# Optimization experiments

Hardware: AMD Instinct MI355X
Metric: run time of the kernel (lower is better)

Reference implementation:

```python
import jax, jax.numpy as jnp
import numpy as np
from jax import lax

DN = ('NCHW', 'OIHW', 'NCHW')

def conv(x, k):
    return lax.conv_general_dilated(x, k, (1, 1), 'SAME', dimension_numbers=DN)

def conv_adj(y, k):
    # adjoint of SAME stride-1 conv: correlate with spatially-flipped, channel-transposed kernel
    return conv(y, jnp.flip(k, (2, 3)).transpose(1, 0, 2, 3))

def setup_inputs() -> dict:
    key = jax.random.key(0)
    ks = jax.random.split(key, 8)
    B, H, W = 8, 512, 512
    Cw, Ch = 4, 32
    return {
        'sino': jax.random.normal(ks[0], (B, 1, H, W), jnp.float32),
        'x': jax.random.normal(ks[1], (B, 1, H, W), jnp.float32),
        'laam': jnp.asarray([0.05], jnp.float32),
        'miu': jnp.asarray([0.01], jnp.float32),
        'Kw': jax.random.normal(ks[2], (Cw, 1, 3, 3), jnp.float32) * 0.1,
        'Ka': jax.random.normal(ks[3], (1, 1, 5, 5), jnp.float32) * 0.1,
        'W1': jax.random.normal(ks[4], (Ch, 1, 3, 3), jnp.float32) * 0.05,
        'b1': jnp.zeros((Ch,), jnp.float32),
        'W2': jax.random.normal(ks[5], (Ch, Ch, 3, 3), jnp.float32) * 0.05,
        'b2': jnp.zeros((Ch,), jnp.float32),
        'W3': jax.random.normal(ks[6], (1, Ch, 3, 3), jnp.float32) * 0.05,
        'b3': jnp.zeros((1,), jnp.float32),
    }

def reference(sino, x, laam, miu, Kw, Ka, W1, b1, W2, b2, W3, b3):
    mu = miu  # shape (1,), broadcasts as scalar

    def Wop(u):  return conv(u, Kw)          # analysis transform, [B,Cw,H,W]
    def WTop(v): return conv_adj(v, Kw)      # synthesis (adjoint)
    def Aop(u):  return conv(u, Ka)          # system operator surrogate
    def ATop(s): return conv_adj(s, Ka)

    def cnn(u):
        h = jax.nn.relu(conv(u, W1) + b1[None, :, None, None])
        h = jax.nn.relu(conv(h, W2) + b2[None, :, None, None])
        return u + conv(h, W3) + b3[None, :, None, None]

    def AWx(p):  # (A^T A + mu W^T W) p
        return ATop(Aop(p)) + mu * WTop(Wop(p))

    # --- MetaInvH forward ---
    Wu = Wop(x)
    dnz = jax.nn.relu(Wu - laam) - jax.nn.relu(-Wu - laam)  # soft threshold
    rhs = ATop(sino) + WTop(dnz) * miu
    uk0 = cnn(x)
    res = AWx(uk0) - rhs

    # --- CG_alg, 5 iterations + final half step ---
    xk, r, p = uk0, res, -res
    for _ in range(5):
        Ap = Aop(p)                                   # [B,1,H,W]
        Wp = Wop(p)                                   # [B,Cw,H,W]
        pATAp = jnp.sum(Ap * Ap, axis=(1, 2, 3))      # [B]
        pWTWp = mu * jnp.sum(Wp * Wp, axis=(1, 2, 3)) # [B]
        rTr = jnp.sum(r * r, axis=(1, 2, 3))
        al = (rTr / (pWTWp + pATAp))[:, None, None, None]
        xk = xk + al * p
        r = r + al * (ATop(Ap) + mu * WTop(Wp))
        be = (jnp.sum(r * r, axis=(1, 2, 3)) / rTr)[:, None, None, None]
        p = -r + be * p
    Ap = Aop(p)
    Wp = Wop(p)
    pATAp = jnp.sum(Ap * Ap, axis=(1, 2, 3))
    pWTWp = mu * jnp.sum(Wp * Wp, axis=(1, 2, 3))
    rTr = jnp.sum(r * r, axis=(1, 2, 3))
    al = (rTr / (pWTWp + pATAp))[:, None, None, None]
    return xk + al * p
```

## Files before the change

### kernel.cpp

```cpp
#include <hip/hip_runtime.h>

#define HH 512
#define WW 512
#define BB 8
#define IMG (HH*WW)
#define NTOT (BB*IMG)

typedef float f32x4 __attribute__((ext_vector_type(4)));
typedef _Float16 half8 __attribute__((ext_vector_type(8)));

__device__ inline uint f2h2(float a, float b) {
  uint d; asm("v_cvt_pkrtz_f16_f32 %0, %1, %2" : "=v"(d) : "v"(a), "v"(b)); return d;
}
__device__ inline uint pkfma(uint a, uint b, uint c) {
  uint d; asm("v_pk_fma_f16 %0, %1, %2, %3" : "=v"(d) : "v"(a), "v"(b), "v"(c)); return d;
}
__device__ inline uint pkmax0(uint a) {
  uint d, z = 0u; asm("v_pk_max_f16 %0, %1, %2" : "=v"(d) : "v"(a), "v"(z)); return d;
}

__device__ inline void atomic_block_sum(float part, float* red, float* dst) {
  for (int off = 32; off > 0; off >>= 1) part += __shfl_down(part, off, 64);
  int lane = threadIdx.x & 63, w = threadIdx.x >> 6;
  if (lane == 0) red[w] = part;
  __syncthreads();
  if (threadIdx.x == 0) atomicAdd(dst, red[0] + red[1] + red[2] + red[3]);
}

__device__ inline bool mA5(int t, int e) {
  return (t==0) ? (e<=2) : (t==1) ? (e<=3) : (t==3) ? (e>=1) : (t==4) ? (e>=2) : true;
}
__device__ inline bool mW3(int t, int e) {
  return (t==0) ? (e<=1) : (t==4) ? (e>=1) : true;
}

__global__ void k_prep(const float* __restrict__ Ka, const float* __restrict__ Kw,
                       const float* __restrict__ miu,
                       const float* __restrict__ W1, const float* __restrict__ b1,
                       const float* __restrict__ W2, const float* __restrict__ W3,
                       float* __restrict__ tab, ushort* __restrict__ w2pk,
                       uint* __restrict__ w1pk, uint* __restrict__ b1pk,
                       ushort* __restrict__ w3fr, float* __restrict__ scal) {
  __shared__ float lka[25], lkw[36], lw1[288], lw3[288];
  int tid = threadIdx.x;
  if (tid < 192) scal[tid] = 0.f;
  if (tid < 25) lka[tid] = Ka[tid];
  if (tid < 36) lkw[tid] = Kw[tid];
  if (tid < 288) { lw1[tid] = W1[tid]; lw3[tid] = W3[tid]; }
  __syncthreads();
  const float mu = miu[0];
  #pragma unroll
  for (int k = 0; k < 2; k++) {
    int idx = tid + k*1024;
    if (idx < 2025) {
      int c = idx / 81, o = idx - c*81;
      int ty = c / 5, tx = c - 5*ty;
      int uy = o / 9 - 4, ux = o % 9 - 4;
      float s = 0.f;
      for (int ey = 0; ey < 5; ey++)
        for (int ex = 0; ex < 5; ex++) {
          int dy = ey + uy, dx = ex + ux;
          if (dy >= 0 && dy < 5 && dx >= 0 && dx < 5 && mA5(ty,ey) && mA5(tx,ex))
            s += lka[ey*5+ex] * lka[dy*5+dx];
        }
      float sw = 0.f;
      for (int ch = 0; ch < 4; ch++)
        for (int ey = 0; ey < 3; ey++)
          for (int ex = 0; ex < 3; ex++) {
            int dy = ey + uy, dx = ex + ux;
            if (dy >= 0 && dy < 3 && dx >= 0 && dx < 3 && mW3(ty,ey) && mW3(tx,ex))
              sw += lkw[ch*9+ey*3+ex] * lkw[ch*9+dy*3+dx];
          }
      tab[idx] = s + mu * sw;
    }
  }
  #pragma unroll
  for (int k = 0; k < 9; k++) {
    int i = tid + k*1024;
    int j = i & 7, l = (i >> 3) & 63, f = i >> 9;
    int t5 = f >> 1, h = f & 1;
    int co = 16*h + (l & 15), ci = 8*(l >> 4) + j;
    w2pk[i] = (ushort)(f2h2(W2[(co*32 + ci)*9 + t5], 0.f) & 0xffffu);
  }
  if (tid < 144) {
    int cp = tid / 9, t = tid % 9;
    w1pk[tid] = f2h2(lw1[(2*cp)*9 + t], lw1[(2*cp+1)*9 + t]);
  }
  if (tid < 16) b1pk[tid] = f2h2(b1[2*tid], b1[2*tid+1]);
  if (tid < 512) {
    int j = tid & 7, l = tid >> 3;
    int tap = l & 15, ch = 8*(l >> 4) + j;
    w3fr[tid] = (tap < 9) ? (ushort)(f2h2(lw3[ch*9 + tap], 0.f) & 0xffffu) : (ushort)0;
  }
}

__launch_bounds__(512)
__global__ void k_cnn(const float* __restrict__ x,
                      const ushort* __restrict__ w2pk, const uint* __restrict__ w1pk,
                      const uint* __restrict__ b1pk, const ushort* __restrict__ w3fr,
                      const float* __restrict__ b2, const float* __restrict__ b3,
                      float* __restrict__ xk) {
  __shared__ __align__(16) uint  h1u[7040];
  __shared__ __align__(16) uint  h2u[5472];
  uint* xs_h2 = h2u;

  const int tid = threadIdx.x;
  const int bimg = blockIdx.z;
  const int oy0 = blockIdx.y * 16, ox0 = blockIdx.x * 16;
  const float* xim = x + (size_t)bimg * IMG;

  for (int i = tid; i < 528; i += 512) {
    int ly = i / 24, lx = i % 24;
    int gy = oy0 + ly - 3, gx = ox0 + lx - 4;
    float v = 0.f;
    if ((unsigned)gy < HH && (unsigned)gx < WW) v = xim[gy*WW + gx];
    xs_h2[i] = f2h2(v, v);
  }
  __syncthreads();

  {
    const int cp = tid & 15;
    const int sg = tid >> 4;
    uint w1r[9];
    #pragma unroll
    for (int k = 0; k < 9; k++) w1r[k] = w1pk[cp*9 + k];
    const uint b1v = b1pk[cp];
    const int kg = cp >> 2, cl = cp & 3;
    #pragma unroll 1
    for (int s = sg; s < 100; s += 32) {
      int row = s / 5, st = s - 5*row;
      int px0 = st * 4;
      uint acc0 = b1v, acc1 = b1v, acc2 = b1v, acc3 = b1v;
      #pragma unroll
      for (int ky = 0; ky < 3; ky++) {
        int base = (row + ky) * 24 + px0;
        uint4 xa = *(const uint4*)&xs_h2[base];
        uint4 xb = *(const uint4*)&xs_h2[base + 4];
        uint xu[8] = {xa.x, xa.y, xa.z, xa.w, xb.x, xb.y, xb.z, xb.w};
        #pragma unroll
        for (int kx = 0; kx < 3; kx++) {
          uint w = w1r[ky*3 + kx];
          acc0 = pkfma(w, xu[1 + kx], acc0);
          acc1 = pkfma(w, xu[2 + kx], acc1);
          acc2 = pkfma(w, xu[3 + kx], acc2);
          acc3 = pkfma(w, xu[4 + kx], acc3);
        }
      }
      int Y = oy0 + row - 2;
      bool rin = (unsigned)Y < HH;
      int ob = row*352 + kg*88 + px0*4 + cl;
      #pragma unroll
      for (int i = 0; i < 4; i++) {
        int X = ox0 + px0 + i - 2;
        uint v = (rin && (unsigned)X < WW) ?
                 pkmax0(i == 0 ? acc0 : (i == 1 ? acc1 : (i == 2 ? acc2 : acc3))) : 0u;
        h1u[ob + i*4] = v;
      }
    }
  }
  __syncthreads();

  const int wv = tid >> 6, lane = tid & 63;
  const int nn = lane & 15, kg = lane >> 4;
  {
    half8 afr[9][2];
    #pragma unroll
    for (int t5 = 0; t5 < 9; t5++) {
      afr[t5][0] = ((const half8*)w2pk)[(t5*2 + 0)*64 + lane];
      afr[t5][1] = ((const half8*)w2pk)[(t5*2 + 1)*64 + lane];
    }
    float b2A[4], b2B[4];
    #pragma unroll
    for (int j = 0; j < 4; j++) { b2A[j] = b2[4*kg + j]; b2B[j] = b2[16 + 4*kg + j]; }

    #pragma unroll 1
    for (int t = wv; t < 27; t += 8) {
      int rp = t / 3, cs = t - 3*rp;
      int tx0 = (cs == 2) ? 10 : (cs << 3);
      int brow = 2*rp + (nn >> 3);
      int bcol = tx0 + (nn & 7);
      f32x4 accA = {0.f,0.f,0.f,0.f}, accB = {0.f,0.f,0.f,0.f};
      #pragma unroll
      for (int ky = 0; ky < 3; ky++)
        #pragma unroll
        for (int kx = 0; kx < 3; kx++) {
          const half8 bfr = *(const half8*)&h1u[(brow+ky)*352 + kg*88 + (bcol+kx)*4];
          accA = __builtin_amdgcn_mfma_f32_16x16x32_f16(afr[ky*3+kx][0], bfr, accA, 0, 0, 0);
          accB = __builtin_amdgcn_mfma_f32_16x16x32_f16(afr[ky*3+kx][1], bfr, accB, 0, 0, 0);
        }
      int gy = oy0 + brow - 1, gx = ox0 + bcol - 1;
      bool inb = ((unsigned)gy < HH) && ((unsigned)gx < WW);
      float v0 = inb ? fmaxf(accA[0] + b2A[0], 0.f) : 0.f;
      float v1 = inb ? fmaxf(accA[1] + b2A[1], 0.f) : 0.f;
      float v2 = inb ? fmaxf(accA[2] + b2A[2], 0.f) : 0.f;
      float v3 = inb ? fmaxf(accA[3] + b2A[3], 0.f) : 0.f;
      uint2 uA = make_uint2(f2h2(v0, v1), f2h2(v2, v3));
      v0 = inb ? fmaxf(accB[0] + b2B[0], 0.f) : 0.f;
      v1 = inb ? fmaxf(accB[1] + b2B[1], 0.f) : 0.f;
      v2 = inb ? fmaxf(accB[2] + b2B[2], 0.f) : 0.f;
      v3 = inb ? fmaxf(accB[3] + b2B[3], 0.f) : 0.f;
      uint2 uB = make_uint2(f2h2(v0, v1), f2h2(v2, v3));
      int base = brow*304 + bcol*4 + (kg & 1)*2;
      *(uint2*)&h2u[base + (kg >> 1)*76]       = uA;
      *(uint2*)&h2u[base + (2 + (kg >> 1))*76] = uB;
    }
  }
  __syncthreads();

  float* Tlds = (float*)h1u;
  {
    const half8 w3f = ((const half8*)w3fr)[lane];
    const int tap = nn;
    #pragma unroll 1
    for (int t = wv; t < 27; t += 8) {
      int rp = t / 3, cs = t - 3*rp;
      int tx0 = (cs == 2) ? 10 : (cs << 3);
      int ay = 2*rp + (nn >> 3);
      int ax = tx0 + (nn & 7);
      const half8 afrag = *(const half8*)&h2u[ay*304 + kg*76 + ax*4];
      f32x4 z = {0.f,0.f,0.f,0.f};
      f32x4 T4 = __builtin_amdgcn_mfma_f32_16x16x32_f16(afrag, w3f, z, 0, 0, 0);
      if (tap < 9) {
        int ty = 2*rp + (kg >> 1);
        int txb = tx0 + 4*(kg & 1);
        float* dst = &Tlds[ty*180 + tap*20 + txb];
        if (cs == 2) {
          dst[0] = T4[0]; dst[1] = T4[1]; dst[2] = T4[2]; dst[3] = T4[3];
        } else {
          *(f32x4*)dst = T4;
        }
      }
    }
  }
  __syncthreads();

  {
    const int half = tid & 1, px = tid >> 1;
    const int oy = px >> 4, ox = px & 15;
    float s = 0.f;
    if (half == 0) {
      #pragma unroll
      for (int t = 0; t < 4; t++)
        s += Tlds[(oy + t/3)*180 + t*20 + (ox + t%3)];
    } else {
      #pragma unroll
      for (int t = 4; t < 9; t++)
        s += Tlds[(oy + t/3)*180 + t*20 + (ox + t%3)];
    }
    float other = __shfl_xor(s, 1, 64);
    if (half == 0) {
      float tot = s + other + b3[0] + xim[(size_t)(oy0+oy)*WW + ox0 + ox];
      xk[(size_t)bimg*IMG + (size_t)(oy0+oy)*WW + ox0 + ox] = tot;
    }
  }
}

__device__ __forceinline__ void apply_M2(const float (*ssrc)[76], float* bandv,
    const float* Gs, const float* __restrict__ tab,
    int tid, int oy0, int ox0, float* accv) {
  const int sy = tid >> 3, sx0 = (tid & 7) * 8;
  #pragma unroll
  for (int k = 0; k < 8; k++) accv[k] = 0.f;
  #pragma unroll 1
  for (int oyy = 0; oyy < 9; oyy++) {
    float g[9];
    #pragma unroll
    for (int t = 0; t < 9; t++) g[t] = Gs[oyy*9+t];
    const float* row = &ssrc[sy+oyy][sx0];
    float4 r0 = *(const float4*)(row);
    float4 r1 = *(const float4*)(row+4);
    float4 r2 = *(const float4*)(row+8);
    float4 r3 = *(const float4*)(row+12);
    float v[16] = {r0.x,r0.y,r0.z,r0.w, r1.x,r1.y,r1.z,r1.w,
                   r2.x,r2.y,r2.z,r2.w, r3.x,r3.y,r3.z,r3.w};
    #pragma unroll
    for (int k = 0; k < 8; k++) {
      float a = accv[k];
      #pragma unroll
      for (int t = 0; t < 9; t++) a = fmaf(g[t], v[k+t], a);
      accv[k] = a;
    }
  }
  const int by = blockIdx.y, bx = blockIdx.x;
  const bool eT = (by == 0), eB = (by == (int)gridDim.y - 1);
  const bool eL = (bx == 0), eR = (bx == (int)gridDim.x - 1);
  if (eT | eB | eL | eR) {
    const int nTop = eT ? 128 : 0;
    const int nBot = eB ? 128 : 0;
    const int yl = eT ? 2 : 0, yh = eB ? 30 : 32;
    const int nL = eL ? 2*(yh-yl) : 0;
    const int nR = eR ? 2*(yh-yl) : 0;
    const int nBand = nTop + nBot + nL + nR;
    if (tid < nBand) {
      int i = tid, bsy, bsx;
      if (i < nTop) { bsy = i >> 6; bsx = i & 63; }
      else if (i < nTop + nBot) { i -= nTop; bsy = 30 + (i >> 6); bsx = i & 63; }
      else if (i < nTop + nBot + nL) { i -= nTop + nBot; bsy = yl + (i >> 1); bsx = i & 1; }
      else { i -= nTop + nBot + nL; bsy = yl + (i >> 1); bsx = 62 + (i & 1); }
      const int gy = oy0 + bsy, gx = ox0 + bsx;
      int ty = (gy == 0) ? 0 : (gy == 1) ? 1 : (gy == HH-1) ? 4 : (gy == HH-2) ? 3 : 2;
      int tx = (gx == 0) ? 0 : (gx == 1) ? 1 : (gx == WW-1) ? 4 : (gx == WW-2) ? 3 : 2;
      const float* S = tab + (ty*5 + tx)*81;
      float a = 0.f;
      #pragma unroll
      for (int oy = 0; oy < 9; oy++) {
        float s0 = S[oy*9+0], s1 = S[oy*9+1], s2 = S[oy*9+2];
        float s3 = S[oy*9+3], s4 = S[oy*9+4], s5 = S[oy*9+5];
        float s6 = S[oy*9+6], s7 = S[oy*9+7], s8 = S[oy*9+8];
        const float* r = &ssrc[bsy+oy][bsx];
        a = fmaf(s0, r[0], a); a = fmaf(s1, r[1], a); a = fmaf(s2, r[2], a);
        a = fmaf(s3, r[3], a); a = fmaf(s4, r[4], a); a = fmaf(s5, r[5], a);
        a = fmaf(s6, r[6], a); a = fmaf(s7, r[7], a); a = fmaf(s8, r[8], a);
      }
      bandv[tid] = a;
    }
    __syncthreads();
    #pragma unroll
    for (int k = 0; k < 8; k++) {
      const int sx = sx0 + k;
      const int gy = oy0 + sy, gx = ox0 + sx;
      if ((gy < 2) || (gy >= HH-2) || (gx < 2) || (gx >= WW-2)) {
        int idx;
        if (eT && sy < 2) idx = sy*64 + sx;
        else if (eB && sy >= 30) idx = nTop + (sy-30)*64 + sx;
        else if (eL && sx < 2) idx = nTop + nBot + (sy-yl)*2 + sx;
        else idx = nTop + nBot + nL + (sy-yl)*2 + (sx-62);
        accv[k] = bandv[idx];
      }
    }
  }
}

__launch_bounds__(256)
__global__ void k_M0(const float* __restrict__ xk, const float* __restrict__ sino,
                     const float* __restrict__ x,
                     float* __restrict__ outR, float* __restrict__ outP,
                     const float* __restrict__ tab,
                     const float* __restrict__ Ka, const float* __restrict__ Kw,
                     const float* __restrict__ laam, const float* __restrict__ miu,
                     float* __restrict__ rtrOut) {
  __shared__ __align__(16) float ssrc[40][76];
  __shared__ __align__(16) float tbuf[36][68];
  __shared__ __align__(16) float ssin[36][68];
  __shared__ __align__(16) float sx[36][68];
  __shared__ float Gs[81], kas[25], kws[36];
  __shared__ float red[4];
  const int tid = threadIdx.x;
  const int bimg = blockIdx.z;
  const int oy0 = blockIdx.y*32, ox0 = blockIdx.x*64;
  if (tid < 81) Gs[tid] = tab[972 + tid];
  if (tid >= 81 && tid < 106) kas[tid-81] = Ka[tid-81];
  if (tid >= 106 && tid < 142) kws[tid-106] = Kw[tid-106];
  const float mu = miu[0];
  const float lam = laam[0];
  const float* sxk = xk + (size_t)bimg*IMG;
  const float* ssi = sino + (size_t)bimg*IMG;
  const float* sxi = x + (size_t)bimg*IMG;

  for (int i = tid; i < 40*76; i += 256) {
    int ly = i/76, lx = i%76;
    int gy = oy0 + ly - 4, gx = ox0 + lx - 4;
    bool in = (lx < 72) && (gy >= 0 && gy < HH && gx >= 0 && gx < WW);
    ssrc[ly][lx] = in ? sxk[gy*WW+gx] : 0.f;
  }
  for (int i = tid; i < 36*68; i += 256) {
    int ly = i/68, lx = i%68;
    int gy = oy0 + ly - 2, gx = ox0 + lx - 2;
    bool in = (gy >= 0 && gy < HH && gx >= 0 && gx < WW);
    ssin[ly][lx] = in ? ssi[gy*WW+gx] : 0.f;
    sx[ly][lx]   = in ? sxi[gy*WW+gx] : 0.f;
  }
  __syncthreads();

  float accv[8];
  apply_M2(ssrc, &tbuf[0][0], Gs, tab, tid, oy0, ox0, accv);

  const int sy = tid >> 3, sx0 = (tid & 7) * 8;
  float rhsv[8];
  #pragma unroll
  for (int k = 0; k < 8; k++) rhsv[k] = 0.f;
  {
    #pragma unroll
    for (int dy = 0; dy < 5; dy++) {
      const float* row = &ssin[sy+4-dy][sx0];
      float4 r0 = *(const float4*)(row);
      float4 r1 = *(const float4*)(row+4);
      float4 r2 = *(const float4*)(row+8);
      float w[12] = {r0.x,r0.y,r0.z,r0.w, r1.x,r1.y,r1.z,r1.w, r2.x,r2.y,r2.z,r2.w};
      #pragma unroll
      for (int k = 0; k < 8; k++)
        #pragma unroll
        for (int dx = 0; dx < 5; dx++)
          rhsv[k] = fmaf(kas[dy*5+dx], w[k+4-dx], rhsv[k]);
    }
  }
  #pragma unroll 1
  for (int ch = 0; ch < 4; ch++) {
    __syncthreads();
    {
      float kw[9];
      #pragma unroll
      for (int k = 0; k < 9; k++) kw[k] = kws[ch*9 + k];
      #pragma unroll 1
      for (int item = tid; item < 2244; item += 256) {
        int dy = item / 66, dx = item - 66*dy;
        int gy = oy0 + dy - 1, gx = ox0 + dx - 1;
        float v = 0.f;
        if (gy >= 0 && gy < HH && gx >= 0 && gx < WW) {
          float wu = 0.f;
          #pragma unroll
          for (int e = 0; e < 9; e++) wu = fmaf(kw[e], sx[dy + e/3][dx + e%3], wu);
          v = fmaxf(wu - lam, 0.f) - fmaxf(-wu - lam, 0.f);
        }
        tbuf[dy][dx] = v;
      }
    }
    __syncthreads();
    {
      float kw[9];
      #pragma unroll
      for (int k = 0; k < 9; k++) kw[k] = mu * kws[ch*9 + k];
      #pragma unroll
      for (int dy = 0; dy < 3; dy++) {
        const float* row = &tbuf[sy+2-dy][sx0];
        float4 r0 = *(const float4*)(row);
        float4 r1 = *(const float4*)(row+4);
        float4 r2 = *(const float4*)(row+8);
        float w[12] = {r0.x,r0.y,r0.z,r0.w, r1.x,r1.y,r1.z,r1.w, r2.x,r2.y,r2.z,r2.w};
        #pragma unroll
        for (int k = 0; k < 8; k++)
          #pragma unroll
          for (int dx = 0; dx < 3; dx++)
            rhsv[k] = fmaf(kw[dy*3+dx], w[k+2-dx], rhsv[k]);
      }
    }
  }

  const int gy = oy0 + sy, gx0 = ox0 + sx0;
  float part = 0.f;
  #pragma unroll
  for (int k = 0; k < 8; k++) {
    size_t idx = (size_t)bimg*IMG + gy*WW + gx0 + k;
    float rv = accv[k] - rhsv[k];
    outR[idx] = rv;
    outP[idx] = -rv;
    part += rv*rv;
  }
  atomic_block_sum(part, red, &rtrOut[bimg]);
}

template<int MODE>
__launch_bounds__(256)
__global__ void k_M(const float* __restrict__ srcA, const float* __restrict__ srcB,
                    float* __restrict__ outQ, float* __restrict__ outP,
                    const float* __restrict__ tab,
                    const float* __restrict__ miu,
                    const float* __restrict__ beN, const float* __restrict__ beD,
                    float* __restrict__ acc, float* __restrict__ rqOut,
                    float* __restrict__ qqOut) {
  __shared__ __align__(16) float ssrc[40][76];
  __shared__ float bandv[256];
  __shared__ float Gs[81];
  __shared__ float red[12];
  const int tid = threadIdx.x;
  const int bimg = blockIdx.z;
  const int oy0 = blockIdx.y*32, ox0 = blockIdx.x*64;
  if (tid < 81) Gs[tid] = tab[972 + tid];
  float be = 0.f;
  if (MODE == 2) be = beN[bimg] / beD[bimg];
  const float* sA = srcA + (size_t)bimg*IMG;
  const float* sB = (MODE == 2) ? srcB + (size_t)bimg*IMG : nullptr;

  for (int i = tid; i < 40*76; i += 256) {
    int ly = i/76, lx = i%76;
    int gy = oy0 + ly - 4, gx = ox0 + lx - 4;
    bool in = (lx < 72) && (gy >= 0 && gy < HH && gx >= 0 && gx < WW);
    float v = 0.f;
    if (MODE == 2) {
      if (in) {
        v = -sA[gy*WW+gx] + be * sB[gy*WW+gx];
        if (ly >= 4 && ly < 36 && lx >= 4 && lx < 68)
          outP[(size_t)bimg*IMG + gy*WW + gx] = v;
      }
    } else {
      if (in) v = sA[gy*WW+gx];
    }
    ssrc[ly][lx] = v;
  }
  __syncthreads();

  float accv[8];
  apply_M2(ssrc, bandv, Gs, tab, tid, oy0, ox0, accv);

  const int sy = tid >> 3, sx0 = (tid & 7) * 8;
  const int gy = oy0 + sy, gx0 = ox0 + sx0;
  if (MODE == 1) {
    float pq = 0.f, qq = 0.f;
    #pragma unroll
    for (int k = 0; k < 8; k++) {
      size_t idx = (size_t)bimg*IMG + gy*WW + gx0 + k;
      float pv = ssrc[sy+4][sx0+4+k];
      float qv = accv[k];
      outQ[idx] = qv;
      pq += pv * qv;
      qq += qv * qv;
    }
    for (int off = 32; off > 0; off >>= 1) {
      pq += __shfl_down(pq, off, 64);
      qq += __shfl_down(qq, off, 64);
    }
    int lane = tid & 63, w = tid >> 6;
    if (lane == 0) { red[w*2] = pq; red[w*2+1] = qq; }
    __syncthreads();
    if (tid == 0) {
      float A = red[0]+red[2]+red[4]+red[6];
      float Q = red[1]+red[3]+red[5]+red[7];
      atomicAdd(&acc[bimg], A);
      if (rqOut) atomicAdd(&rqOut[bimg], -A);
      if (qqOut) atomicAdd(&qqOut[bimg], Q);
    }
  } else {
    float part = 0.f;
    #pragma unroll
    for (int k = 0; k < 8; k++) {
      size_t idx = (size_t)bimg*IMG + gy*WW + gx0 + k;
      float pv = ssrc[sy+4][sx0+4+k];
      outQ[idx] = accv[k];
      part += pv * accv[k];
    }
    atomic_block_sum(part, red, &acc[bimg]);
  }
}

__launch_bounds__(256)
__global__ void k_it(float* __restrict__ xk,
                     const float* __restrict__ rold, float* __restrict__ rnew,
                     const float* __restrict__ pold, float* __restrict__ pnew,
                     const float* __restrict__ qold, float* __restrict__ qnew,
                     const float* __restrict__ tab,
                     float* __restrict__ scal, int it, int storeQ) {
  __shared__ __align__(16) float ssrc[40][76];
  __shared__ float rlds[2048];
  __shared__ float bandv[256];
  __shared__ float Gs[81];
  __shared__ float red[12];
  const int tid = threadIdx.x;
  const int bimg = blockIdx.z;
  const int oy0 = blockIdx.y*32, ox0 = blockIdx.x*64;
  if (tid < 81) Gs[tid] = tab[972 + tid];
  const float den_p = scal[       (it-1)*8 + bimg];
  const float rq_p  = scal[ 48 + (it-1)*8 + bimg];
  const float qq_p  = scal[ 96 + (it-1)*8 + bimg];
  const float rtr_p = scal[144 + (it-1)*8 + bimg];
  const float al = rtr_p / den_p;
  const float rtr_c = fmaf(al, fmaf(al, qq_p, 2.f*rq_p), rtr_p);
  const float be = rtr_c / rtr_p;
  if (tid == 0) scal[144 + it*8 + bimg] = rtr_c;
  const size_t ib = (size_t)bimg*IMG;

  for (int i = tid; i < 40*76; i += 256) {
    int ly = i/76, lx = i%76;
    int gy = oy0 + ly - 4, gx = ox0 + lx - 4;
    bool in = (lx < 72) && (gy >= 0 && gy < HH && gx >= 0 && gx < WW);
    float v = 0.f;
    if (in) {
      size_t g = ib + (size_t)gy*WW + gx;
      float pg = pold[g];
      float rn = fmaf(al, qold[g], rold[g]);
      v = fmaf(be, pg, -rn);
      if (ly >= 4 && ly < 36 && lx >= 4 && lx < 68) {
        pnew[g] = v;
        rnew[g] = rn;
        xk[g] = fmaf(al, pg, xk[g]);
        rlds[(ly-4)*64 + (lx-4)] = rn;
      }
    }
    ssrc[ly][lx] = v;
  }
  __syncthreads();

  float accv[8];
  apply_M2(ssrc, bandv, Gs, tab, tid, oy0, ox0, accv);

  const int sy = tid >> 3, sx0 = (tid & 7) * 8;
  const int gy = oy0 + sy, gx0 = ox0 + sx0;
  float s_den = 0.f, s_rq = 0.f, s_qq = 0.f;
  #pragma unroll
  for (int k = 0; k < 8; k++) {
    size_t idx = ib + (size_t)gy*WW + gx0 + k;
    float qv = accv[k];
    float pv = ssrc[sy+4][sx0+4+k];
    float rv = rlds[sy*64 + sx0 + k];
    if (storeQ) qnew[idx] = qv;
    s_den += pv*qv;
    s_rq  += rv*qv;
    s_qq  += qv*qv;
  }
  for (int off = 32; off > 0; off >>= 1) {
    s_den += __shfl_down(s_den, off, 64);
    s_rq  += __shfl_down(s_rq,  off, 64);
    s_qq  += __shfl_down(s_qq,  off, 64);
  }
  int lane = tid & 63, w = tid >> 6;
  if (lane == 0) { red[w*3] = s_den; red[w*3+1] = s_rq; red[w*3+2] = s_qq; }
  __syncthreads();
  if (tid == 0) {
    atomicAdd(&scal[       it*8 + bimg], red[0]+red[3]+red[6]+red[9]);
    atomicAdd(&scal[ 48 + it*8 + bimg], red[1]+red[4]+red[7]+red[10]);
    atomicAdd(&scal[ 96 + it*8 + bimg], red[2]+red[5]+red[8]+red[11]);
  }
}

__launch_bounds__(256)
__global__ void k_upd(float* __restrict__ xk, float* __restrict__ r,
                      const float* __restrict__ p, const float* __restrict__ q,
                      const float* __restrict__ num, const float* __restrict__ den,
                      float* __restrict__ rtrOut) {
  __shared__ float red[4];
  const int tid = threadIdx.x;
  const int bimg = blockIdx.x >> 8;
  const size_t idx4 = (size_t)blockIdx.x * 256 + tid;
  const float al = num[bimg] / den[bimg];
  float4 xv = ((const float4*)xk)[idx4];
  float4 pv = ((const float4*)p)[idx4];
  float4 rv = ((const float4*)r)[idx4];
  float4 qv = ((const float4*)q)[idx4];
  xv.x += al*pv.x; xv.y += al*pv.y; xv.z += al*pv.z; xv.w += al*pv.w;
  rv.x += al*qv.x; rv.y += al*qv.y; rv.z += al*qv.z; rv.w += al*qv.w;
  ((float4*)xk)[idx4] = xv;
  ((float4*)r)[idx4] = rv;
  float part = rv.x*rv.x + rv.y*rv.y + rv.z*rv.z + rv.w*rv.w;
  atomic_block_sum(part, red, &rtrOut[bimg]);
}

__launch_bounds__(256)
__global__ void k_final(const float* __restrict__ xk, const float* __restrict__ p,
                        const float* __restrict__ num, const float* __restrict__ den,
                        float* __restrict__ out) {
  const int tid = threadIdx.x;
  const int bimg = blockIdx.x >> 8;
  const size_t idx4 = (size_t)blockIdx.x * 256 + tid;
  const float al = num[bimg] / den[bimg];
  float4 xv = ((const float4*)xk)[idx4];
  float4 pv = ((const float4*)p)[idx4];
  float4 o;
  o.x = xv.x + al*pv.x; o.y = xv.y + al*pv.y; o.z = xv.z + al*pv.z; o.w = xv.w + al*pv.w;
  ((float4*)out)[idx4] = o;
}

extern "C" void kernel_launch(void* const* d_in, const int* in_sizes, int n_in,
                              void* d_out, int out_size, void* d_ws, size_t ws_size,
                              hipStream_t stream) {
  const float* sino = (const float*)d_in[0];
  const float* x    = (const float*)d_in[1];
  const float* laam = (const float*)d_in[2];
  const float* miu  = (const float*)d_in[3];
  const float* Kw   = (const float*)d_in[4];
  const float* Ka   = (const float*)d_in[5];
  const float* W1   = (const float*)d_in[6];
  const float* b1   = (const float*)d_in[7];
  const float* W2   = (const float*)d_in[8];
  const float* b2   = (const float*)d_in[9];
  const float* W3   = (const float*)d_in[10];
  const float* b3   = (const float*)d_in[11];

  const bool fused = ws_size >= (size_t)6*NTOT*4 + 65536;
  float* ws = (float*)d_ws;
  const size_t nb = fused ? 6 : 5;
  float* tail = ws + nb*(size_t)NTOT;
  float* tab  = tail;
  float* scal = tail + 2048;
  ushort* w2pk = (ushort*)(scal + 192);
  uint*   w1pk = (uint*)(w2pk + 9216);
  uint*   b1pk = w1pk + 144;
  ushort* w3fr = (ushort*)(b1pk + 16);
  float* dout = (float*)d_out;

  k_prep<<<1, 1024, 0, stream>>>(Ka, Kw, miu, W1, b1, W2, W3, tab, w2pk, w1pk,
                                 b1pk, w3fr, scal);

  float* xk = ws;
  k_cnn<<<dim3(32,32,8), 512, 0, stream>>>(x, w2pk, w1pk, b1pk, w3fr, b2, b3, xk);

  dim3 mg(8,16,8);
  if (fused) {
    float* rA = ws + (size_t)NTOT;
    float* rB = ws + 2*(size_t)NTOT;
    float* pA = ws + 3*(size_t)NTOT;
    float* pB = ws + 4*(size_t)NTOT;
    float* qB = ws + 5*(size_t)NTOT;
    float* qA = dout;
    k_M0<<<mg,256,0,stream>>>(xk, sino, x, rA, pA, tab, Ka, Kw, laam, miu, &scal[144]);
    k_M<1><<<mg,256,0,stream>>>(pA, nullptr, qA, nullptr, tab, miu,
                                nullptr, nullptr, &scal[0], &scal[48], &scal[96]);
    float *rc=rA, *rn=rB, *pc=pA, *pn=pB, *qc=qA, *qn=qB;
    for (int it = 1; it <= 5; it++) {
      k_it<<<mg,256,0,stream>>>(xk, rc, rn, pc, pn, qc, qn, tab, scal,
                                it, it < 5 ? 1 : 0);
      float* t;
      t = rc; rc = rn; rn = t;
      t = pc; pc = pn; pn = t;
      t = qc; qc = qn; qn = t;
    }
    k_final<<<2048,256,0,stream>>>(xk, pc, &scal[144+40], &scal[40], dout);
  } else {
    float* r  = ws + (size_t)NTOT;
    float* p0 = ws + 2*(size_t)NTOT;
    float* p1 = ws + 3*(size_t)NTOT;
    float* q  = ws + 4*(size_t)NTOT;
    k_M0<<<mg,256,0,stream>>>(xk, sino, x, r, p0, tab, Ka, Kw, laam, miu, &scal[144]);
    k_M<1><<<mg,256,0,stream>>>(p0, nullptr, q, nullptr, tab, miu,
                                nullptr, nullptr, &scal[0], nullptr, nullptr);
    k_upd<<<2048,256,0,stream>>>(xk, r, p0, q, &scal[144], &scal[0], &scal[144+8]);
    float* pcur = p0; float* pnext = p1;
    for (int i = 1; i <= 4; i++) {
      k_M<2><<<mg,256,0,stream>>>(r, pcur, q, pnext, tab, miu,
                                  &scal[144+8*i], &scal[144+8*(i-1)], &scal[8*i],
                                  nullptr, nullptr);
      k_upd<<<2048,256,0,stream>>>(xk, r, pnext, q, &scal[144+8*i], &scal[8*i],
                                   &scal[144+8*(i+1)]);
      float* t = pcur; pcur = pnext; pnext = t;
    }
    k_M<2><<<mg,256,0,stream>>>(r, pcur, q, pnext, tab, miu,
                                &scal[144+40], &scal[144+32], &scal[40],
                                nullptr, nullptr);
    k_final<<<2048,256,0,stream>>>(xk, pnext, &scal[144+40], &scal[40], dout);
  }
}
```

Baseline: 389.1 us.

## Fuse CG iterations into a persistent kernel with grid barriers

```diff
diff --git a/kernel.cpp b/kernel.cpp
--- a/kernel.cpp
+++ b/kernel.cpp
@@ -25,6 +25,35 @@
   if (lane == 0) red[w] = part;
   __syncthreads();
   if (threadIdx.x == 0) atomicAdd(dst, red[0] + red[1] + red[2] + red[3]);
+}
+
+__device__ inline void reduce3_atomic(float a, float b, float c, float* red,
+                                      float* da, float* db, float* dc) {
+  for (int off = 32; off > 0; off >>= 1) {
+    a += __shfl_down(a, off, 64);
+    b += __shfl_down(b, off, 64);
+    c += __shfl_down(c, off, 64);
+  }
+  int lane = threadIdx.x & 63, w = threadIdx.x >> 6;
+  if (lane == 0) { red[w*3] = a; red[w*3+1] = b; red[w*3+2] = c; }
+  __syncthreads();
+  if (threadIdx.x == 0) {
+    atomicAdd(da, red[0]+red[3]+red[6]+red[9]);
+    if (db) atomicAdd(db, red[1]+red[4]+red[7]+red[10]);
+    if (dc) atomicAdd(dc, red[2]+red[5]+red[8]+red[11]);
+  }
+}
+
+__device__ inline void gbar(uint* cnt, uint target) {
+  __syncthreads();
+  if (threadIdx.x == 0) {
+    __threadfence();
+    __hip_atomic_fetch_add(cnt, 1u, __ATOMIC_ACQ_REL, __HIP_MEMORY_SCOPE_AGENT);
+    while (__hip_atomic_load(cnt, __ATOMIC_ACQUIRE, __HIP_MEMORY_SCOPE_AGENT) < target)
+      __builtin_amdgcn_s_sleep(8);
+  }
+  __syncthreads();
+  __threadfence();
 }
 
 __device__ inline bool mA5(int t, int e) {
@@ -43,7 +72,7 @@
                        ushort* __restrict__ w3fr, float* __restrict__ scal) {
   __shared__ float lka[25], lkw[36], lw1[288], lw3[288];
   int tid = threadIdx.x;
-  if (tid < 192) scal[tid] = 0.f;
+  if (tid < 256) scal[tid] = 0.f;
   if (tid < 25) lka[tid] = Ka[tid];
   if (tid < 36) lkw[tid] = Kw[tid];
   if (tid < 288) { lw1[tid] = W1[tid]; lw3[tid] = W3[tid]; }
@@ -304,13 +333,9 @@
       float a = 0.f;
       #pragma unroll
       for (int oy = 0; oy < 9; oy++) {
-        float s0 = S[oy*9+0], s1 = S[oy*9+1], s2 = S[oy*9+2];
-        float s3 = S[oy*9+3], s4 = S[oy*9+4], s5 = S[oy*9+5];
-        float s6 = S[oy*9+6], s7 = S[oy*9+7], s8 = S[oy*9+8];
         const float* r = &ssrc[bsy+oy][bsx];
-        a = fmaf(s0, r[0], a); a = fmaf(s1, r[1], a); a = fmaf(s2, r[2], a);
-        a = fmaf(s3, r[3], a); a = fmaf(s4, r[4], a); a = fmaf(s5, r[5], a);
-        a = fmaf(s6, r[6], a); a = fmaf(s7, r[7], a); a = fmaf(s8, r[8], a);
+        #pragma unroll
+        for (int ox = 0; ox < 9; ox++) a = fmaf(S[oy*9+ox], r[ox], a);
       }
       bandv[tid] = a;
     }
@@ -449,12 +474,232 @@
   atomic_block_sum(part, red, &rtrOut[bimg]);
 }
 
+__device__ inline void stage_frame64(float (*ssrc)[76], const float* __restrict__ src,
+                                     size_t ib, int oy0, int ox0, int tid) {
+  for (int i = tid; i < 1376; i += 256) {
+    int ly, lx;
+    if (i < 304) { ly = i/76; lx = i - 76*ly; }
+    else if (i < 608) { int j = i-304; int q = j/76; ly = 68 + q; lx = j - 76*q; }
+    else { int j = i-608; int q = j/12; ly = 4 + q; int c = j - 12*q; lx = (c < 4) ? c : 64 + c; }
+    int gy = oy0 + ly - 4, gx = ox0 + lx - 4;
+    float v = 0.f;
+    if (lx < 72 && (unsigned)gy < HH && (unsigned)gx < WW)
+      v = src[ib + (size_t)gy*WW + gx];
+    ssrc[ly][lx] = v;
+  }
+}
+
+__device__ inline void apply_cg(const float (*ssrc)[76], float* bandv,
+    const float* Gs, const float* __restrict__ tab,
+    int tid, int oy0, int ox0, int by, int bx, float (*q16)[8]) {
+  const int sy = tid >> 3, sx0 = (tid & 7) * 8;
+  #pragma unroll
+  for (int s = 0; s < 2; s++) {
+    #pragma unroll
+    for (int k = 0; k < 8; k++) q16[s][k] = 0.f;
+    const int R = sy + 32*s;
+    #pragma unroll 1
+    for (int oyy = 0; oyy < 9; oyy++) {
+      float g[9];
+      #pragma unroll
+      for (int t = 0; t < 9; t++) g[t] = Gs[oyy*9+t];
+      const float* row = &ssrc[R+oyy][sx0];
+      float4 r0 = *(const float4*)(row);
+      float4 r1 = *(const float4*)(row+4);
+      float4 r2 = *(const float4*)(row+8);
+      float4 r3 = *(const float4*)(row+12);
+      float v[16] = {r0.x,r0.y,r0.z,r0.w, r1.x,r1.y,r1.z,r1.w,
+                     r2.x,r2.y,r2.z,r2.w, r3.x,r3.y,r3.z,r3.w};
+      #pragma unroll
+      for (int k = 0; k < 8; k++) {
+        float a = q16[s][k];
+        #pragma unroll
+        for (int t = 0; t < 9; t++) a = fmaf(g[t], v[k+t], a);
+        q16[s][k] = a;
+      }
+    }
+  }
+  const bool eT = (by == 0), eB = (by == 7);
+  const bool eL = (bx == 0), eR = (bx == 7);
+  if (eT | eB | eL | eR) {
+    const int nTop = eT ? 128 : 0;
+    const int nBot = eB ? 128 : 0;
+    const int yl = eT ? 2 : 0, yh = eB ? 62 : 64;
+    const int nL = eL ? 2*(yh-yl) : 0;
+    const int nR = eR ? 2*(yh-yl) : 0;
+    const int nBand = nTop + nBot + nL + nR;
+    if (tid < nBand) {
+      int i = tid, bsy, bsx;
+      if (i < nTop) { bsy = i >> 6; bsx = i & 63; }
+      else if (i < nTop + nBot) { i -= nTop; bsy = 62 + (i >> 6); bsx = i & 63; }
+      else if (i < nTop + nBot + nL) { i -= nTop + nBot; bsy = yl + (i >> 1); bsx = i & 1; }
+      else { i -= nTop + nBot + nL; bsy = yl + (i >> 1); bsx = 62 + (i & 1); }
+      const int gy = oy0 + bsy, gx = ox0 + bsx;
+      int ty = (gy == 0) ? 0 : (gy == 1) ? 1 : (gy == HH-1) ? 4 : (gy == HH-2) ? 3 : 2;
+      int tx = (gx == 0) ? 0 : (gx == 1) ? 1 : (gx == WW-1) ? 4 : (gx == WW-2) ? 3 : 2;
+      const float* S = tab + (ty*5 + tx)*81;
+      float a = 0.f;
+      #pragma unroll
+      for (int oy = 0; oy < 9; oy++) {
+        const float* r = &ssrc[bsy+oy][bsx];
+        #pragma unroll
+        for (int ox = 0; ox < 9; ox++) a = fmaf(S[oy*9+ox], r[ox], a);
+      }
+      bandv[tid] = a;
+    }
+    __syncthreads();
+    #pragma unroll
+    for (int s = 0; s < 2; s++) {
+      const int R = sy + 32*s;
+      const int gy = oy0 + R;
+      #pragma unroll
+      for (int k = 0; k < 8; k++) {
+        const int sx = sx0 + k;
+        const int gx = ox0 + sx;
+        if ((gy < 2) || (gy >= HH-2) || (gx < 2) || (gx >= WW-2)) {
+          int idx;
+          if (eT && R < 2) idx = R*64 + sx;
+          else if (eB && R >= 62) idx = nTop + (R-62)*64 + sx;
+          else if (eL && sx < 2) idx = nTop + nBot + (R-yl)*2 + sx;
+          else idx = nTop + nBot + nL + (R-yl)*2 + (sx-62);
+          q16[s][k] = bandv[idx];
+        }
+      }
+    }
+  }
+}
+
+__launch_bounds__(256, 2)
+__global__ void k_cg(const float* __restrict__ xk0, const float* __restrict__ rA,
+                     const float* __restrict__ pA, float* __restrict__ pg,
+                     const float* __restrict__ tab, float* __restrict__ scal,
+                     uint* __restrict__ bar, float* __restrict__ dout) {
+  __shared__ __align__(16) float ssrc[72][76];
+  __shared__ float bandv[256];
+  __shared__ float Gs[81];
+  __shared__ float red[12];
+  const int tid = threadIdx.x;
+  const int bx = blockIdx.x, by = blockIdx.y, bimg = blockIdx.z;
+  const int oy0 = by*64, ox0 = bx*64;
+  if (tid < 81) Gs[tid] = tab[972 + tid];
+  const size_t ib = (size_t)bimg*IMG;
+  const int sy = tid >> 3, sx0v = (tid & 7)*8;
+  const size_t base0 = ib + (size_t)(oy0+sy)*WW + ox0 + sx0v;
+  const size_t base1 = base0 + (size_t)32*WW;
+  uint nb = 0;
+
+  float xk16[2][8], r16[2][8], p16[2][8], q16[2][8];
+  {
+    float4 a0 = *(const float4*)&xk0[base0];
+    float4 a1 = *(const float4*)&xk0[base0+4];
+    float4 a2 = *(const float4*)&xk0[base1];
+    float4 a3 = *(const float4*)&xk0[base1+4];
+    xk16[0][0]=a0.x; xk16[0][1]=a0.y; xk16[0][2]=a0.z; xk16[0][3]=a0.w;
+    xk16[0][4]=a1.x; xk16[0][5]=a1.y; xk16[0][6]=a1.z; xk16[0][7]=a1.w;
+    xk16[1][0]=a2.x; xk16[1][1]=a2.y; xk16[1][2]=a2.z; xk16[1][3]=a2.w;
+    xk16[1][4]=a3.x; xk16[1][5]=a3.y; xk16[1][6]=a3.z; xk16[1][7]=a3.w;
+    float4 b0 = *(const float4*)&rA[base0];
+    float4 b1 = *(const float4*)&rA[base0+4];
+    float4 b2 = *(const float4*)&rA[base1];
+    float4 b3 = *(const float4*)&rA[base1+4];
+    r16[0][0]=b0.x; r16[0][1]=b0.y; r16[0][2]=b0.z; r16[0][3]=b0.w;
+    r16[0][4]=b1.x; r16[0][5]=b1.y; r16[0][6]=b1.z; r16[0][7]=b1.w;
+    r16[1][0]=b2.x; r16[1][1]=b2.y; r16[1][2]=b2.z; r16[1][3]=b2.w;
+    r16[1][4]=b3.x; r16[1][5]=b3.y; r16[1][6]=b3.z; r16[1][7]=b3.w;
+    #pragma unroll
+    for (int s = 0; s < 2; s++)
+      #pragma unroll
+      for (int k = 0; k < 8; k++) p16[s][k] = -r16[s][k];
+  }
+
+  stage_frame64(ssrc, pA, ib, oy0, ox0, tid);
+  #pragma unroll
+  for (int s = 0; s < 2; s++)
+    #pragma unroll
+    for (int k = 0; k < 8; k++) ssrc[sy + 32*s + 4][sx0v + 4 + k] = p16[s][k];
+  __syncthreads();
+  apply_cg(ssrc, bandv, Gs, tab, tid, oy0, ox0, by, bx, q16);
+  {
+    float sd = 0.f, sq = 0.f;
+    #pragma unroll
+    for (int s = 0; s < 2; s++)
+      #pragma unroll
+      for (int k = 0; k < 8; k++) { sd += p16[s][k]*q16[s][k]; sq += q16[s][k]*q16[s][k]; }
+    reduce3_atomic(sd, sq, 0.f, red, &scal[bimg], &scal[96+bimg], nullptr);
+  }
+  gbar(bar, (++nb)*512u);
+  float den_p = __hip_atomic_load(&scal[bimg],     __ATOMIC_RELAXED, __HIP_MEMORY_SCOPE_AGENT);
+  float qq_p  = __hip_atomic_load(&scal[96+bimg],  __ATOMIC_RELAXED, __HIP_MEMORY_SCOPE_AGENT);
+  float rtr_p = __hip_atomic_load(&scal[144+bimg], __ATOMIC_RELAXED, __HIP_MEMORY_SCOPE_AGENT);
+  float rq_p  = -den_p;
+
+  #pragma unroll 1
+  for (int it = 1; it <= 5; ++it) {
+    const float al = rtr_p / den_p;
+    const float rtr_c = fmaf(al, fmaf(al, qq_p, 2.f*rq_p), rtr_p);
+    const float be = rtr_c / rtr_p;
+    #pragma unroll
+    for (int s = 0; s < 2; s++)
+      #pragma unroll
+      for (int k = 0; k < 8; k++) {
+        xk16[s][k] = fmaf(al, p16[s][k], xk16[s][k]);
+        r16[s][k]  = fmaf(al, q16[s][k], r16[s][k]);
+        p16[s][k]  = fmaf(be, p16[s][k], -r16[s][k]);
+      }
+    *(float4*)&pg[base0]   = make_float4(p16[0][0], p16[0][1], p16[0][2], p16[0][3]);
+    *(float4*)&pg[base0+4] = make_float4(p16[0][4], p16[0][5], p16[0][6], p16[0][7]);
+    *(float4*)&pg[base1]   = make_float4(p16[1][0], p16[1][1], p16[1][2], p16[1][3]);
+    *(float4*)&pg[base1+4] = make_float4(p16[1][4], p16[1][5], p16[1][6], p16[1][7]);
+    gbar(bar, (++nb)*512u);
+    stage_frame64(ssrc, pg, ib, oy0, ox0, tid);
+    #pragma unroll
+    for (int s = 0; s < 2; s++)
+      #pragma unroll
+      for (int k = 0; k < 8; k++) ssrc[sy + 32*s + 4][sx0v + 4 + k] = p16[s][k];
+    __syncthreads();
+    apply_cg(ssrc, bandv, Gs, tab, tid, oy0, ox0, by, bx, q16);
+    {
+      float sd = 0.f, sr = 0.f, sq = 0.f;
+      #pragma unroll
+      for (int s = 0; s < 2; s++)
+        #pragma unroll
+        for (int k = 0; k < 8; k++) {
+          sd += p16[s][k]*q16[s][k];
+          sr += r16[s][k]*q16[s][k];
+          sq += q16[s][k]*q16[s][k];
+        }
+      reduce3_atomic(sd, sr, sq, red, &scal[it*8+bimg], &scal[48+it*8+bimg],
+                     &scal[96+it*8+bimg]);
+    }
+    gbar(bar, (++nb)*512u);
+    den_p = __hip_atomic_load(&scal[it*8+bimg],    __ATOMIC_RELAXED, __HIP_MEMORY_SCOPE_AGENT);
+    rq_p  = __hip_atomic_load(&scal[48+it*8+bimg], __ATOMIC_RELAXED, __HIP_MEMORY_SCOPE_AGENT);
+    qq_p  = __hip_atomic_load(&scal[96+it*8+bimg], __ATOMIC_RELAXED, __HIP_MEMORY_SCOPE_AGENT);
+    rtr_p = rtr_c;
+  }
+
+  {
+    const float al = rtr_p / den_p;
+    *(float4*)&dout[base0] = make_float4(
+      fmaf(al,p16[0][0],xk16[0][0]), fmaf(al,p16[0][1],xk16[0][1]),
+      fmaf(al,p16[0][2],xk16[0][2]), fmaf(al,p16[0][3],xk16[0][3]));
+    *(float4*)&dout[base0+4] = make_float4(
+      fmaf(al,p16[0][4],xk16[0][4]), fmaf(al,p16[0][5],xk16[0][5]),
+      fmaf(al,p16[0][6],xk16[0][6]), fmaf(al,p16[0][7],xk16[0][7]));
+    *(float4*)&dout[base1] = make_float4(
+      fmaf(al,p16[1][0],xk16[1][0]), fmaf(al,p16[1][1],xk16[1][1]),
+      fmaf(al,p16[1][2],xk16[1][2]), fmaf(al,p16[1][3],xk16[1][3]));
+    *(float4*)&dout[base1+4] = make_float4(
+      fmaf(al,p16[1][4],xk16[1][4]), fmaf(al,p16[1][5],xk16[1][5]),
+      fmaf(al,p16[1][6],xk16[1][6]), fmaf(al,p16[1][7],xk16[1][7]));
+  }
+}
+
 template<int MODE>
 __launch_bounds__(256)
 __global__ void k_M(const float* __restrict__ srcA, const float* __restrict__ srcB,
                     float* __restrict__ outQ, float* __restrict__ outP,
                     const float* __restrict__ tab,
-                    const float* __restrict__ miu,
                     const float* __restrict__ beN, const float* __restrict__ beD,
                     float* __restrict__ acc, float* __restrict__ rqOut,
                     float* __restrict__ qqOut) {
@@ -505,20 +750,8 @@
       pq += pv * qv;
       qq += qv * qv;
     }
-    for (int off = 32; off > 0; off >>= 1) {
-      pq += __shfl_down(pq, off, 64);
-      qq += __shfl_down(qq, off, 64);
-    }
-    int lane = tid & 63, w = tid >> 6;
-    if (lane == 0) { red[w*2] = pq; red[w*2+1] = qq; }
-    __syncthreads();
-    if (tid == 0) {
-      float A = red[0]+red[2]+red[4]+red[6];
-      float Q = red[1]+red[3]+red[5]+red[7];
-      atomicAdd(&acc[bimg], A);
-      if (rqOut) atomicAdd(&rqOut[bimg], -A);
-      if (qqOut) atomicAdd(&qqOut[bimg], Q);
-    }
+    reduce3_atomic(pq, -pq, qq, red, &acc[bimg], rqOut ? &rqOut[bimg] : nullptr,
+                   qqOut ? &qqOut[bimg] : nullptr);
   } else {
     float part = 0.f;
     #pragma unroll
@@ -565,13 +798,13 @@
     float v = 0.f;
     if (in) {
       size_t g = ib + (size_t)gy*WW + gx;
-      float pg = pold[g];
+      float pgv = pold[g];
       float rn = fmaf(al, qold[g], rold[g]);
-      v = fmaf(be, pg, -rn);
+      v = fmaf(be, pgv, -rn);
       if (ly >= 4 && ly < 36 && lx >= 4 && lx < 68) {
         pnew[g] = v;
         rnew[g] = rn;
-        xk[g] = fmaf(al, pg, xk[g]);
+        xk[g] = fmaf(al, pgv, xk[g]);
         rlds[(ly-4)*64 + (lx-4)] = rn;
       }
     }
@@ -596,41 +829,8 @@
     s_rq  += rv*qv;
     s_qq  += qv*qv;
   }
-  for (int off = 32; off > 0; off >>= 1) {
-    s_den += __shfl_down(s_den, off, 64);
-    s_rq  += __shfl_down(s_rq,  off, 64);
-    s_qq  += __shfl_down(s_qq,  off, 64);
-  }
-  int lane = tid & 63, w = tid >> 6;
-  if (lane == 0) { red[w*3] = s_den; red[w*3+1] = s_rq; red[w*3+2] = s_qq; }
-  __syncthreads();
-  if (tid == 0) {
-    atomicAdd(&scal[       it*8 + bimg], red[0]+red[3]+red[6]+red[9]);
-    atomicAdd(&scal[ 48 + it*8 + bimg], red[1]+red[4]+red[7]+red[10]);
-    atomicAdd(&scal[ 96 + it*8 + bimg], red[2]+red[5]+red[8]+red[11]);
-  }
-}
-
-__launch_bounds__(256)
-__global__ void k_upd(float* __restrict__ xk, float* __restrict__ r,
-                      const float* __restrict__ p, const float* __restrict__ q,
-                      const float* __restrict__ num, const float* __restrict__ den,
-                      float* __restrict__ rtrOut) {
-  __shared__ float red[4];
-  const int tid = threadIdx.x;
-  const int bimg = blockIdx.x >> 8;
-  const size_t idx4 = (size_t)blockIdx.x * 256 + tid;
-  const float al = num[bimg] / den[bimg];
-  float4 xv = ((const float4*)xk)[idx4];
-  float4 pv = ((const float4*)p)[idx4];
-  float4 rv = ((const float4*)r)[idx4];
-  float4 qv = ((const float4*)q)[idx4];
-  xv.x += al*pv.x; xv.y += al*pv.y; xv.z += al*pv.z; xv.w += al*pv.w;
-  rv.x += al*qv.x; rv.y += al*qv.y; rv.z += al*qv.z; rv.w += al*qv.w;
-  ((float4*)xk)[idx4] = xv;
-  ((float4*)r)[idx4] = rv;
-  float part = rv.x*rv.x + rv.y*rv.y + rv.z*rv.z + rv.w*rv.w;
-  atomic_block_sum(part, red, &rtrOut[bimg]);
+  reduce3_atomic(s_den, s_rq, s_qq, red, &scal[it*8+bimg], &scal[48+it*8+bimg],
+                 &scal[96+it*8+bimg]);
 }
 
 __launch_bounds__(256)
@@ -664,18 +864,21 @@
   const float* W3   = (const float*)d_in[10];
   const float* b3   = (const float*)d_in[11];
 
-  const bool fused = ws_size >= (size_t)6*NTOT*4 + 65536;
   float* ws = (float*)d_ws;
-  const size_t nb = fused ? 6 : 5;
-  float* tail = ws + nb*(size_t)NTOT;
+  float* tail = ws + (size_t)6*NTOT;
   float* tab  = tail;
   float* scal = tail + 2048;
-  ushort* w2pk = (ushort*)(scal + 192);
+  uint*  bar  = (uint*)(scal + 192);
+  ushort* w2pk = (ushort*)(scal + 256);
   uint*   w1pk = (uint*)(w2pk + 9216);
   uint*   b1pk = w1pk + 144;
   ushort* w3fr = (ushort*)(b1pk + 16);
   float* dout = (float*)d_out;
 
+  int nbOcc = 0;
+  (void)hipOccupancyMaxActiveBlocksPerMultiprocessor(&nbOcc, k_cg, 256, 0);
+  const bool persistent = (nbOcc >= 2);
+
   k_prep<<<1, 1024, 0, stream>>>(Ka, Kw, miu, W1, b1, W2, W3, tab, w2pk, w1pk,
                                  b1pk, w3fr, scal);
 
@@ -683,17 +886,20 @@
   k_cnn<<<dim3(32,32,8), 512, 0, stream>>>(x, w2pk, w1pk, b1pk, w3fr, b2, b3, xk);
 
   dim3 mg(8,16,8);
-  if (fused) {
-    float* rA = ws + (size_t)NTOT;
-    float* rB = ws + 2*(size_t)NTOT;
-    float* pA = ws + 3*(size_t)NTOT;
+  float* rA = ws + (size_t)NTOT;
+  float* pA = ws + 2*(size_t)NTOT;
+  float* pg = ws + 3*(size_t)NTOT;
+  k_M0<<<mg,256,0,stream>>>(xk, sino, x, rA, pA, tab, Ka, Kw, laam, miu, &scal[144]);
+
+  if (persistent) {
+    k_cg<<<dim3(8,8,8), 256, 0, stream>>>(xk, rA, pA, pg, tab, scal, bar, dout);
+  } else {
     float* pB = ws + 4*(size_t)NTOT;
     float* qB = ws + 5*(size_t)NTOT;
     float* qA = dout;
-    k_M0<<<mg,256,0,stream>>>(xk, sino, x, rA, pA, tab, Ka, Kw, laam, miu, &scal[144]);
-    k_M<1><<<mg,256,0,stream>>>(pA, nullptr, qA, nullptr, tab, miu,
+    k_M<1><<<mg,256,0,stream>>>(pA, nullptr, qA, nullptr, tab,
                                 nullptr, nullptr, &scal[0], &scal[48], &scal[96]);
-    float *rc=rA, *rn=rB, *pc=pA, *pn=pB, *qc=qA, *qn=qB;
+    float *rc=rA, *rn=pg, *pc=pA, *pn=pB, *qc=qA, *qn=qB;
     for (int it = 1; it <= 5; it++) {
       k_it<<<mg,256,0,stream>>>(xk, rc, rn, pc, pn, qc, qn, tab, scal,
                                 it, it < 5 ? 1 : 0);
@@ -703,27 +909,5 @@
       t = qc; qc = qn; qn = t;
     }
     k_final<<<2048,256,0,stream>>>(xk, pc, &scal[144+40], &scal[40], dout);
-  } else {
-    float* r  = ws + (size_t)NTOT;
-    float* p0 = ws + 2*(size_t)NTOT;
-    float* p1 = ws + 3*(size_t)NTOT;
-    float* q  = ws + 4*(size_t)NTOT;
-    k_M0<<<mg,256,0,stream>>>(xk, sino, x, r, p0, tab, Ka, Kw, laam, miu, &scal[144]);
-    k_M<1><<<mg,256,0,stream>>>(p0, nullptr, q, nullptr, tab, miu,
-                                nullptr, nullptr, &scal[0], nullptr, nullptr);
-    k_upd<<<2048,256,0,stream>>>(xk, r, p0, q, &scal[144], &scal[0], &scal[144+8]);
-    float* pcur = p0; float* pnext = p1;
-    for (int i = 1; i <= 4; i++) {
-      k_M<2><<<mg,256,0,stream>>>(r, pcur, q, pnext, tab, miu,
-                                  &scal[144+8*i], &scal[144+8*(i-1)], &scal[8*i],
-                                  nullptr, nullptr);
-      k_upd<<<2048,256,0,stream>>>(xk, r, pnext, q, &scal[144+8*i], &scal[8*i],
-                                   &scal[144+8*(i+1)]);
-      float* t = pcur; pcur = pnext; pnext = t;
-    }
-    k_M<2><<<mg,256,0,stream>>>(r, pcur, q, pnext, tab, miu,
-                                &scal[144+40], &scal[144+32], &scal[40],
-                                nullptr, nullptr);
-    k_final<<<2048,256,0,stream>>>(xk, pnext, &scal[144+40], &scal[40], dout);
-  }
-}
+  }
+}
```

Result: no change. 389.5 us (+0.1%).
